# Kernel optimization log

Hardware: AMD Instinct MI355X
Metric: run time of the kernel (lower is better)

Reference implementation:

```python
import jax, jax.numpy as jnp
import numpy as np

FP8_MAX = 448.0  # max finite value of float8_e4m3fn


def _fp8_quant(v, scale):
    # emulate saturating scaled cast to float8_e4m3fn, then dequant-free fp8 storage (upcast to f32 for the gemm)
    q = jnp.clip(v / scale, -FP8_MAX, FP8_MAX)
    return q.astype(jnp.float8_e4m3fn).astype(jnp.float32)


def setup_inputs() -> dict:
    key = jax.random.key(0)
    k0, k1, k2, k3 = jax.random.split(key, 4)
    T, H, I, E = 1024, 1024, 2816, 8
    x = jax.random.normal(k0, (T, H), jnp.float32)
    router_logits = jax.random.normal(k1, (T, E), jnp.float32)
    w13_weight = jax.random.normal(k2, (E, 2 * I, H), jnp.float32) * 0.02
    w2_weight = jax.random.normal(k3, (E, H, I), jnp.float32) * 0.02
    return {
        "x": x,
        "router_logits": router_logits,
        "w13_weight": w13_weight,
        "w2_weight": w2_weight,
        "w13_input_scale": jnp.ones((E,), jnp.float32),
        "w2_input_scale": jnp.ones((E,), jnp.float32),
        "top_k": 2,
    }


def reference(x, router_logits, w13_weight, w2_weight, w13_input_scale, w2_input_scale, top_k):
    T, H = x.shape
    E, two_I, _ = w13_weight.shape
    I = two_I // 2

    # --- routing: softmax -> top_k -> renormalize (select_experts) ---
    probs = jax.nn.softmax(router_logits, axis=-1)
    topk_w, topk_ids = jax.lax.top_k(probs, top_k)            # [T,K]
    topk_w = topk_w / jnp.sum(topk_w, axis=-1, keepdims=True)
    # dense combine matrix [T,E]: sparsity of the grouped gemm dispatch
    combine = jnp.zeros((T, E), x.dtype).at[jnp.arange(T)[:, None], topk_ids].add(topk_w)

    # --- per-expert fp8 weight quantization (ops.scaled_fp8_quant per expert) ---
    w13_scale = jnp.max(jnp.abs(w13_weight), axis=(1, 2)) / FP8_MAX  # [E]
    w2_scale = jnp.max(jnp.abs(w2_weight), axis=(1, 2)) / FP8_MAX
    w13_q = _fp8_quant(w13_weight, w13_scale[:, None, None])         # [E,2I,H]
    w2_q = _fp8_quant(w2_weight, w2_scale[:, None, None])            # [E,H,I]

    # --- grouped gemm 1: per-expert activation quant + fp8 gemm + dequant scale ---
    x_q = _fp8_quant(x[None], w13_input_scale[:, None, None])        # [E,T,H]
    h = jnp.einsum('eth,eih->eti', x_q, w13_q) * (w13_input_scale * w13_scale)[:, None, None]

    # --- silu_and_mul: gate = first intermediate_size rows, up = second ---
    act = jax.nn.silu(h[..., :I]) * h[..., I:]                       # [E,T,I]

    # --- grouped gemm 2 ---
    act_q = _fp8_quant(act, w2_input_scale[:, None, None])
    o = jnp.einsum('eti,ehi->eth', act_q, w2_q) * (w2_input_scale * w2_scale)[:, None, None]

    # --- post_reorder: weighted combine of selected experts ---
    return jnp.einsum('te,eth->th', combine, o)                      # [T,H]
```

## Files before the change

kernel.cpp:

```cpp
#include <hip/hip_runtime.h>
#include <cstdint>
#include <cstddef>

#define T_TOK 1024
#define H_DIM 1024
#define I_DIM 2816
#define E_NUM 8
#define PAIRS 2048
#define KSPLIT 4
#define NT1 (I_DIM / 32)
#define AMX2_X 32

typedef __attribute__((ext_vector_type(4))) float f32x4;
typedef __attribute__((ext_vector_type(4))) unsigned int u32x4;
typedef long i64;

__device__ __forceinline__ unsigned char fp8e4m3_sw(float v) {
  v = fminf(448.f, fmaxf(-448.f, v));
  unsigned b = __float_as_uint(v);
  unsigned s = (b >> 24) & 0x80u;
  float a = fabsf(v);
  if (a < 0.015625f) {
    int m = (int)rintf(a * 512.f);
    return (unsigned char)(s | (unsigned)m);
  }
  unsigned ab = b & 0x7fffffffu;
  unsigned rnd = 0x7FFFFu + ((ab >> 20) & 1u);
  ab += rnd;
  int e = (int)(ab >> 23) - 127;
  unsigned m = (ab >> 20) & 7u;
  if (e > 8 || (e == 8 && m > 6)) { e = 8; m = 6; }
  return (unsigned char)(s | (unsigned)((e + 7) << 3) | m);
}

__device__ __forceinline__ unsigned q4(float a, float b, float c, float d) {
#if __has_builtin(__builtin_amdgcn_cvt_pk_fp8_f32)
  unsigned w = (unsigned)__builtin_amdgcn_cvt_pk_fp8_f32(a, b, 0, false);
  return (unsigned)__builtin_amdgcn_cvt_pk_fp8_f32(c, d, (int)w, true);
#else
  return (unsigned)fp8e4m3_sw(a) | ((unsigned)fp8e4m3_sw(b) << 8) |
         ((unsigned)fp8e4m3_sw(c) << 16) | ((unsigned)fp8e4m3_sw(d) << 24);
#endif
}

__device__ __forceinline__ unsigned char q1(float a) {
#if __has_builtin(__builtin_amdgcn_cvt_pk_fp8_f32)
  return (unsigned char)((unsigned)__builtin_amdgcn_cvt_pk_fp8_f32(a, a, 0, false) & 0xFFu);
#else
  return fp8e4m3_sw(a);
#endif
}

__device__ __forceinline__ unsigned q4v(float4 f, float inv) {
  return q4(f.x * inv, f.y * inv, f.z * inv, f.w * inv);
}

__device__ __forceinline__ float wave_max(float m) {
#pragma unroll
  for (int off = 32; off > 0; off >>= 1) m = fmaxf(m, __shfl_xor(m, off));
  return m;
}

__global__ __launch_bounds__(256) void pre_k(const float* __restrict__ w13,
                                             const float* __restrict__ logits,
                                             float* __restrict__ part13,
                                             int* __restrict__ cnt_g,
                                             int* __restrict__ offs_g,
                                             int* __restrict__ pair_tok,
                                             float* __restrict__ pair_w,
                                             int* __restrict__ pairidx) {
  const int tid = threadIdx.x;
  if (blockIdx.x < 1024) {
    const int e = blockIdx.x >> 7, sub = blockIdx.x & 127;
    const float4* src = (const float4*)w13 + (size_t)e * (2 * I_DIM * H_DIM / 4);
    int idx = sub * 256 + tid;
    const int stride = 128 * 256;
    float m = 0.f;
#pragma unroll
    for (int j = 0; j < 44; j += 4) {
      float4 v0 = src[idx + (size_t)(j + 0) * stride];
      float4 v1 = src[idx + (size_t)(j + 1) * stride];
      float4 v2 = src[idx + (size_t)(j + 2) * stride];
      float4 v3 = src[idx + (size_t)(j + 3) * stride];
      m = fmaxf(m, fmaxf(fmaxf(fabsf(v0.x), fabsf(v0.y)), fmaxf(fabsf(v0.z), fabsf(v0.w))));
      m = fmaxf(m, fmaxf(fmaxf(fabsf(v1.x), fabsf(v1.y)), fmaxf(fabsf(v1.z), fabsf(v1.w))));
      m = fmaxf(m, fmaxf(fmaxf(fabsf(v2.x), fabsf(v2.y)), fmaxf(fabsf(v2.z), fabsf(v2.w))));
      m = fmaxf(m, fmaxf(fmaxf(fabsf(v3.x), fabsf(v3.y)), fmaxf(fabsf(v3.z), fabsf(v3.w))));
    }
    m = wave_max(m);
    __shared__ float wmax[4];
    int lane = tid & 63, wid = tid >> 6;
    if (lane == 0) wmax[wid] = m;
    __syncthreads();
    if (tid == 0)
      part13[blockIdx.x] = fmaxf(fmaxf(wmax[0], wmax[1]), fmaxf(wmax[2], wmax[3]));
    return;
  }

  __shared__ int cnt_s[E_NUM], pos_s[E_NUM];
  if (tid < E_NUM) cnt_s[tid] = 0;
  __syncthreads();
  int i0s[4], i1s[4];
  float w0s[4], w1s[4];
#pragma unroll
  for (int j = 0; j < 4; j++) {
    int t = tid * 4 + j;
    float l[E_NUM];
#pragma unroll
    for (int k = 0; k < E_NUM; k++) l[k] = logits[t * E_NUM + k];
    int i0 = 0; float b0 = l[0];
#pragma unroll
    for (int k = 1; k < E_NUM; k++) { if (l[k] > b0) { b0 = l[k]; i0 = k; } }
    int i1 = -1; float b1 = -3.4e38f;
#pragma unroll
    for (int k = 0; k < E_NUM; k++) { if (k != i0 && l[k] > b1) { b1 = l[k]; i1 = k; } }
    float e1 = expf(b1 - b0);
    float d = 1.f + e1;
    i0s[j] = i0; i1s[j] = i1; w0s[j] = 1.f / d; w1s[j] = e1 / d;
    atomicAdd(&cnt_s[i0], 1);
    atomicAdd(&cnt_s[i1], 1);
  }
  __syncthreads();
  if (tid == 0) {
    int s = 0;
#pragma unroll
    for (int e = 0; e < E_NUM; e++) {
      cnt_g[e] = cnt_s[e];
      offs_g[e] = s;
      pos_s[e] = s;
      s += cnt_s[e];
    }
    offs_g[E_NUM] = s;
  }
  __syncthreads();
#pragma unroll
  for (int j = 0; j < 4; j++) {
    int t = tid * 4 + j;
    int s0 = atomicAdd(&pos_s[i0s[j]], 1);
    pair_tok[s0] = t; pair_w[s0] = w0s[j]; pairidx[2 * t] = s0;
    int s1 = atomicAdd(&pos_s[i1s[j]], 1);
    pair_tok[s1] = t; pair_w[s1] = w1s[j]; pairidx[2 * t + 1] = s1;
  }
}

__global__ __launch_bounds__(256) void quantx_k(const float* __restrict__ x,
                                                const int* __restrict__ pair_tok,
                                                const int* __restrict__ offs,
                                                const float* __restrict__ s13,
                                                unsigned char* __restrict__ Xq) {
  int p = blockIdx.x;
  int t = pair_tok[p];
  int e = 0;
#pragma unroll
  for (int j = 1; j < E_NUM; j++) { if (p >= offs[j]) e = j; }
  float inv = 1.f / s13[e];
  float4 v = ((const float4*)(x + (size_t)t * H_DIM))[threadIdx.x];
  float a = fminf(448.f, fmaxf(-448.f, v.x * inv));
  float b = fminf(448.f, fmaxf(-448.f, v.y * inv));
  float c = fminf(448.f, fmaxf(-448.f, v.z * inv));
  float dd = fminf(448.f, fmaxf(-448.f, v.w * inv));
  ((unsigned*)(Xq + (size_t)p * H_DIM))[threadIdx.x] = q4(a, b, c, dd);
}

__global__ __launch_bounds__(512) void gemm1_k(const float* __restrict__ w13,
                                               const float* __restrict__ w2,
                                               const unsigned char* __restrict__ Xq,
                                               unsigned char* __restrict__ H1,
                                               const int* __restrict__ cnt,
                                               const int* __restrict__ offs,
                                               const float* __restrict__ part13,
                                               float* __restrict__ part2,
                                               const float* __restrict__ s13,
                                               const float* __restrict__ s2in) {
  const int e = blockIdx.z;
  const int tid = threadIdx.x, lane = tid & 63, wq = tid >> 6;

  if (blockIdx.x >= NT1) {
    const int bx2 = (blockIdx.x - NT1) * 4 + blockIdx.y;
    const float4* src = (const float4*)w2 + (size_t)e * (H_DIM * I_DIM / 4);
    int idx = bx2 * 512 + tid;
    const int stride = 128 * 512;
    float m = 0.f;
#pragma unroll
    for (int j = 0; j < 11; j++) {
      float4 v = src[idx + (size_t)j * stride];
      m = fmaxf(m, fmaxf(fmaxf(fabsf(v.x), fabsf(v.y)), fmaxf(fabsf(v.z), fabsf(v.w))));
    }
    m = wave_max(m);
    __shared__ float wmax2[8];
    if (lane == 0) wmax2[wq] = m;
    __syncthreads();
    if (tid == 0) {
      float mm = wmax2[0];
#pragma unroll
      for (int j = 1; j < 8; j++) mm = fmaxf(mm, wmax2[j]);
      part2[e * 128 + bx2] = mm;
    }
    return;
  }

  __shared__ float redA[8];
  {
    float v = part13[e * 128 + (tid & 127)];
    v = wave_max(v);
    if (lane == 0) redA[wq] = v;
  }
  __syncthreads();
  float amax = redA[0];
#pragma unroll
  for (int j = 1; j < 8; j++) amax = fmaxf(amax, redA[j]);

  const int count = cnt[e];
  const int m0 = blockIdx.y * 256;
  if (m0 >= count) return;
  const int nt = blockIdx.x;
  const int base = offs[e];

  const float inv_w = 448.f / amax;
  const float gs = s13[e] * (amax / 448.f);
  const float inv_a2 = 1.f / s2in[e];

  __shared__ __align__(16) unsigned char Bs[64][80];

  const int fr = lane & 15, ks = lane >> 4;

  f32x4 accg[2][2], accu[2][2];
#pragma unroll
  for (int i = 0; i < 2; i++)
#pragma unroll
    for (int j = 0; j < 2; j++) { accg[i][j] = (f32x4)0.f; accu[i][j] = (f32x4)0.f; }

  int rbse = base + m0 + wq * 32 + fr;
  int r0 = rbse;      if (r0 > PAIRS - 1) r0 = PAIRS - 1;
  int r1 = rbse + 16; if (r1 > PAIRS - 1) r1 = PAIRS - 1;
  const unsigned char* a0p = Xq + (size_t)r0 * H_DIM + ks * 8;
  const unsigned char* a1p = Xq + (size_t)r1 * H_DIM + ks * 8;

  const int brow = tid >> 3, bseg = tid & 7;
  const float* b_src = w13 + ((size_t)e * 2 * I_DIM + (size_t)nt * 32 +
                              (brow & 31) + (size_t)(brow >> 5) * I_DIM) * H_DIM + bseg * 8;

  float4 fb0 = ((const float4*)b_src)[0], fb1 = ((const float4*)b_src)[1];
  unsigned qb0 = q4v(fb0, inv_w), qb1 = q4v(fb1, inv_w);
  i64 a00 = *(const i64*)a0p,        a01 = *(const i64*)(a0p + 32);
  i64 a10 = *(const i64*)a1p,        a11 = *(const i64*)(a1p + 32);

  for (int t = 0; t < H_DIM / 64; ++t) {
    __syncthreads();
    ((unsigned*)&Bs[brow][bseg * 8])[0] = qb0;
    ((unsigned*)&Bs[brow][bseg * 8])[1] = qb1;
    __syncthreads();
    i64 c00 = a00, c01 = a01, c10 = a10, c11 = a11;
    if (t + 1 < H_DIM / 64) {
      int k0 = (t + 1) * 64;
      fb0 = ((const float4*)(b_src + k0))[0];
      fb1 = ((const float4*)(b_src + k0))[1];
      a00 = *(const i64*)(a0p + k0); a01 = *(const i64*)(a0p + k0 + 32);
      a10 = *(const i64*)(a1p + k0); a11 = *(const i64*)(a1p + k0 + 32);
    }
#pragma unroll
    for (int kk = 0; kk < 2; kk++) {
      i64 af0 = kk ? c01 : c00;
      i64 af1 = kk ? c11 : c10;
#pragma unroll
      for (int ni = 0; ni < 2; ni++) {
        i64 bg = *(const i64*)&Bs[ni * 16 + fr][kk * 32 + ks * 8];
        i64 bu = *(const i64*)&Bs[32 + ni * 16 + fr][kk * 32 + ks * 8];
        accg[0][ni] = __builtin_amdgcn_mfma_f32_16x16x32_fp8_fp8(af0, bg, accg[0][ni], 0, 0, 0);
        accg[1][ni] = __builtin_amdgcn_mfma_f32_16x16x32_fp8_fp8(af1, bg, accg[1][ni], 0, 0, 0);
        accu[0][ni] = __builtin_amdgcn_mfma_f32_16x16x32_fp8_fp8(af0, bu, accu[0][ni], 0, 0, 0);
        accu[1][ni] = __builtin_amdgcn_mfma_f32_16x16x32_fp8_fp8(af1, bu, accu[1][ni], 0, 0, 0);
      }
    }
    qb0 = q4v(fb0, inv_w);
    qb1 = q4v(fb1, inv_w);
  }

  const int rg = lane >> 4;
#pragma unroll
  for (int mi = 0; mi < 2; mi++) {
#pragma unroll
    for (int rr = 0; rr < 4; rr++) {
      int lrow = wq * 32 + mi * 16 + rg * 4 + rr;
      if (m0 + lrow < count) {
        size_t p = (size_t)(base + m0 + lrow);
#pragma unroll
        for (int ni = 0; ni < 2; ni++) {
          int col = nt * 32 + ni * 16 + fr;
          float g = accg[mi][ni][rr] * gs;
          float u = accu[mi][ni][rr] * gs;
          float act = g / (1.f + expf(-g)) * u * inv_a2;
          act = fminf(448.f, fmaxf(-448.f, act));
          H1[p * I_DIM + col] = q1(act);
        }
      }
    }
  }
}

__global__ __launch_bounds__(512) void gemm2_k(const float* __restrict__ w2,
                                               const unsigned char* __restrict__ H1,
                                               float* __restrict__ Op,
                                               const int* __restrict__ cnt,
                                               const int* __restrict__ offs,
                                               const float* __restrict__ part2,
                                               const float* __restrict__ s2in,
                                               const float* __restrict__ pair_w) {
  const int e = blockIdx.z;
  const int tid = threadIdx.x, lane = tid & 63, wq = tid >> 6;

  __shared__ float redA[8];
  {
    float v = part2[e * 128 + (tid & 127)];
    v = wave_max(v);
    if (lane == 0) redA[wq] = v;
  }
  __syncthreads();
  float amax = redA[0];
#pragma unroll
  for (int j = 1; j < 8; j++) amax = fmaxf(amax, redA[j]);

  const int count = cnt[e];
  const int m0 = blockIdx.y * 128;
  if (m0 >= count) return;
  const int nt = blockIdx.x & 15;
  const int ksp = blockIdx.x >> 4;
  const int n0 = nt * 64;
  const int base = offs[e];

  const float inv_w = 448.f / amax;
  const float s2 = s2in[e] * (amax / 448.f);

  __shared__ __align__(16) unsigned char Bs[64][80];

  const int fr = lane & 15, ks = lane >> 4;

  f32x4 acc[4];
#pragma unroll
  for (int i = 0; i < 4; i++) acc[i] = (f32x4)0.f;

  const int KITER = (I_DIM / 64) / KSPLIT;
  const int kbase = ksp * KITER * 64;

  int rbse = base + m0 + wq * 16 + fr;
  int r0 = rbse; if (r0 > PAIRS - 1) r0 = PAIRS - 1;
  const unsigned char* ap = H1 + (size_t)r0 * I_DIM + kbase + ks * 8;

  const int brow = tid >> 3, bseg = tid & 7;
  const float* b_src = w2 + ((size_t)e * H_DIM + n0 + brow) * I_DIM + kbase + bseg * 8;

  float4 fb0 = ((const float4*)b_src)[0], fb1 = ((const float4*)b_src)[1];
  unsigned qb0 = q4v(fb0, inv_w), qb1 = q4v(fb1, inv_w);
  i64 a0 = *(const i64*)ap, a1 = *(const i64*)(ap + 32);

  for (int t = 0; t < KITER; ++t) {
    __syncthreads();
    ((unsigned*)&Bs[brow][bseg * 8])[0] = qb0;
    ((unsigned*)&Bs[brow][bseg * 8])[1] = qb1;
    __syncthreads();
    i64 c0 = a0, c1 = a1;
    if (t + 1 < KITER) {
      int k0 = (t + 1) * 64;
      fb0 = ((const float4*)(b_src + k0))[0];
      fb1 = ((const float4*)(b_src + k0))[1];
      a0 = *(const i64*)(ap + k0); a1 = *(const i64*)(ap + k0 + 32);
    }
#pragma unroll
    for (int kk = 0; kk < 2; kk++) {
      i64 af = kk ? c1 : c0;
#pragma unroll
      for (int ni = 0; ni < 4; ni++) {
        i64 b = *(const i64*)&Bs[ni * 16 + fr][kk * 32 + ks * 8];
        acc[ni] = __builtin_amdgcn_mfma_f32_16x16x32_fp8_fp8(af, b, acc[ni], 0, 0, 0);
      }
    }
    qb0 = q4v(fb0, inv_w);
    qb1 = q4v(fb1, inv_w);
  }

  const int rg = lane >> 4;
#pragma unroll
  for (int rr = 0; rr < 4; rr++) {
    int lrow = wq * 16 + rg * 4 + rr;
    if (m0 + lrow < count) {
      size_t p = (size_t)(base + m0 + lrow);
      float pw = pair_w[p];
#pragma unroll
      for (int ni = 0; ni < 4; ni++) {
        int col = n0 + ni * 16 + fr;
        Op[((size_t)ksp * PAIRS + p) * H_DIM + col] = acc[ni][rr] * s2 * pw;
      }
    }
  }
}

__global__ __launch_bounds__(256) void combine_k(const float* __restrict__ Op,
                                                 const int* __restrict__ pairidx,
                                                 float* __restrict__ out) {
  int t = blockIdx.x;
  int p0 = pairidx[2 * t], p1 = pairidx[2 * t + 1];
  f32x4 acc = (f32x4)0.f;
#pragma unroll
  for (int s = 0; s < KSPLIT; s++) {
    f32x4 a = ((const f32x4*)(Op + ((size_t)s * PAIRS + p0) * H_DIM))[threadIdx.x];
    f32x4 b = ((const f32x4*)(Op + ((size_t)s * PAIRS + p1) * H_DIM))[threadIdx.x];
    acc += a + b;
  }
  ((f32x4*)(out + (size_t)t * H_DIM))[threadIdx.x] = acc;
}

extern "C" void kernel_launch(void* const* d_in, const int* in_sizes, int n_in,
                              void* d_out, int out_size, void* d_ws, size_t ws_size,
                              hipStream_t stream) {
  (void)in_sizes; (void)n_in; (void)out_size; (void)ws_size;
  const float* x      = (const float*)d_in[0];
  const float* logits = (const float*)d_in[1];
  const float* w13    = (const float*)d_in[2];
  const float* w2     = (const float*)d_in[3];
  const float* s13    = (const float*)d_in[4];
  const float* s2in   = (const float*)d_in[5];
  float* out = (float*)d_out;

  char* ws = (char*)d_ws;
  int* cnt      = (int*)(ws + 128);
  int* offs     = (int*)(ws + 192);
  float* part13 = (float*)(ws + 4096);
  float* part2  = (float*)(ws + 8192);
  int* pair_tok = (int*)(ws + 17408);
  float* pair_w = (float*)(ws + 25600);
  int* pairidx  = (int*)(ws + 33792);
  unsigned char* Xq = (unsigned char*)(ws + (size_t)(1 << 20));
  unsigned char* H1 = (unsigned char*)(ws + (size_t)4 * (1 << 20));
  float* Op         = (float*)(ws + (size_t)10 * (1 << 20));

  pre_k<<<1025, 256, 0, stream>>>(w13, logits, part13, cnt, offs,
                                  pair_tok, pair_w, pairidx);

  quantx_k<<<PAIRS, 256, 0, stream>>>(x, pair_tok, offs, s13, Xq);

  gemm1_k<<<dim3(NT1 + AMX2_X, 4, E_NUM), 512, 0, stream>>>(
      w13, w2, Xq, H1, cnt, offs, part13, part2, s13, s2in);

  gemm2_k<<<dim3(16 * KSPLIT, 8, E_NUM), 512, 0, stream>>>(
      w2, H1, Op, cnt, offs, part2, s2in, pair_w);

  combine_k<<<T_TOK, 256, 0, stream>>>(Op, pairidx, out);
}
```

Measured before the change: 202.8 us.

## Stage fp8 activations through LDS with coalesced loads and retile gemm1 blocks

Both grouped GEMMs now load the fp8 activation tile cooperatively with 16-byte coalesced global loads into shared memory. They then read MFMA fragments from LDS instead of doing scattered 8-byte per-lane global loads. gemm1 moves to 256-thread blocks covering 128 rows instead of 256, and loads gate and up weights separately. A block-index swizzle places the two M halves of the same N tile next to each other so they can share weight reads in L2. The trade-off is more blocks that re-read and re-quantize fp32 weight tiles, plus extra LDS use and LDS traffic.

```diff
diff --git a/kernel.cpp b/kernel.cpp
--- a/kernel.cpp
+++ b/kernel.cpp
@@ -8,7 +8,7 @@
 #define E_NUM 8
 #define PAIRS 2048
 #define KSPLIT 4
-#define NT1 (I_DIM / 32)
+#define NT1 88
 #define AMX2_X 32
 
 typedef __attribute__((ext_vector_type(4))) float f32x4;
@@ -162,7 +162,7 @@
   ((unsigned*)(Xq + (size_t)p * H_DIM))[threadIdx.x] = q4(a, b, c, dd);
 }
 
-__global__ __launch_bounds__(512) void gemm1_k(const float* __restrict__ w13,
+__global__ __launch_bounds__(256) void gemm1_k(const float* __restrict__ w13,
                                                const float* __restrict__ w2,
                                                const unsigned char* __restrict__ Xq,
                                                unsigned char* __restrict__ H1,
@@ -175,51 +175,50 @@
   const int e = blockIdx.z;
   const int tid = threadIdx.x, lane = tid & 63, wq = tid >> 6;
 
-  if (blockIdx.x >= NT1) {
-    const int bx2 = (blockIdx.x - NT1) * 4 + blockIdx.y;
+  if (blockIdx.x >= 2 * NT1) {
+    const int bx2 = (blockIdx.x - 2 * NT1) * 4 + blockIdx.y;
     const float4* src = (const float4*)w2 + (size_t)e * (H_DIM * I_DIM / 4);
-    int idx = bx2 * 512 + tid;
-    const int stride = 128 * 512;
+    int idx = bx2 * 256 + tid;
+    const int stride = 128 * 256;
     float m = 0.f;
 #pragma unroll
-    for (int j = 0; j < 11; j++) {
+    for (int j = 0; j < 22; j++) {
       float4 v = src[idx + (size_t)j * stride];
       m = fmaxf(m, fmaxf(fmaxf(fabsf(v.x), fabsf(v.y)), fmaxf(fabsf(v.z), fabsf(v.w))));
     }
     m = wave_max(m);
-    __shared__ float wmax2[8];
+    __shared__ float wmax2[4];
     if (lane == 0) wmax2[wq] = m;
     __syncthreads();
     if (tid == 0) {
-      float mm = wmax2[0];
-#pragma unroll
-      for (int j = 1; j < 8; j++) mm = fmaxf(mm, wmax2[j]);
+      float mm = fmaxf(fmaxf(wmax2[0], wmax2[1]), fmaxf(wmax2[2], wmax2[3]));
       part2[e * 128 + bx2] = mm;
     }
     return;
   }
 
-  __shared__ float redA[8];
+  __shared__ float redA[4];
   {
     float v = part13[e * 128 + (tid & 127)];
     v = wave_max(v);
     if (lane == 0) redA[wq] = v;
   }
   __syncthreads();
-  float amax = redA[0];
-#pragma unroll
-  for (int j = 1; j < 8; j++) amax = fmaxf(amax, redA[j]);
-
+  float amax = fmaxf(fmaxf(redA[0], redA[1]), fmaxf(redA[2], redA[3]));
+
+  const int bid = blockIdx.x;
+  const int nt = (bid & 7) + (bid >> 4) * 8;
+  const int mhalf = (bid >> 3) & 1;
+  const int m0 = (blockIdx.y * 2 + mhalf) * 128;
   const int count = cnt[e];
-  const int m0 = blockIdx.y * 256;
   if (m0 >= count) return;
-  const int nt = blockIdx.x;
   const int base = offs[e];
 
   const float inv_w = 448.f / amax;
   const float gs = s13[e] * (amax / 448.f);
   const float inv_a2 = 1.f / s2in[e];
 
+  __shared__ __align__(16) unsigned char As[128][80];
   __shared__ __align__(16) unsigned char Bs[64][80];
 
   const int fr = lane & 15, ks = lane >> 4;
@@ -230,50 +229,59 @@
 #pragma unroll
     for (int j = 0; j < 2; j++) { accg[i][j] = (f32x4)0.f; accu[i][j] = (f32x4)0.f; }
 
-  int rbse = base + m0 + wq * 32 + fr;
-  int r0 = rbse;      if (r0 > PAIRS - 1) r0 = PAIRS - 1;
-  int r1 = rbse + 16; if (r1 > PAIRS - 1) r1 = PAIRS - 1;
-  const unsigned char* a0p = Xq + (size_t)r0 * H_DIM + ks * 8;
-  const unsigned char* a1p = Xq + (size_t)r1 * H_DIM + ks * 8;
+  const int ar0 = tid >> 2, aseg = tid & 3;
+  int pr0 = base + m0 + ar0;      if (pr0 > PAIRS - 1) pr0 = PAIRS - 1;
+  int pr1 = base + m0 + ar0 + 64; if (pr1 > PAIRS - 1) pr1 = PAIRS - 1;
+  const unsigned char* a_src0 = Xq + (size_t)pr0 * H_DIM + aseg * 16;
+  const unsigned char* a_src1 = Xq + (size_t)pr1 * H_DIM + aseg * 16;
 
   const int brow = tid >> 3, bseg = tid & 7;
-  const float* b_src = w13 + ((size_t)e * 2 * I_DIM + (size_t)nt * 32 +
-                              (brow & 31) + (size_t)(brow >> 5) * I_DIM) * H_DIM + bseg * 8;
-
-  float4 fb0 = ((const float4*)b_src)[0], fb1 = ((const float4*)b_src)[1];
-  unsigned qb0 = q4v(fb0, inv_w), qb1 = q4v(fb1, inv_w);
-  i64 a00 = *(const i64*)a0p,        a01 = *(const i64*)(a0p + 32);
-  i64 a10 = *(const i64*)a1p,        a11 = *(const i64*)(a1p + 32);
+  const float* bg_src = w13 + ((size_t)e * 2 * I_DIM + (size_t)nt * 32 + brow) * H_DIM + bseg * 8;
+  const float* bu_src = bg_src + (size_t)I_DIM * H_DIM;
+
+  u32x4 ra0 = *(const u32x4*)a_src0;
+  u32x4 ra1 = *(const u32x4*)a_src1;
+  float4 fg0 = ((const float4*)bg_src)[0], fg1 = ((const float4*)bg_src)[1];
+  float4 fu0 = ((const float4*)bu_src)[0], fu1 = ((const float4*)bu_src)[1];
+  unsigned qg0 = q4v(fg0, inv_w), qg1 = q4v(fg1, inv_w);
+  unsigned qu0 = q4v(fu0, inv_w), qu1 = q4v(fu1, inv_w);
 
   for (int t = 0; t < H_DIM / 64; ++t) {
     __syncthreads();
-    ((unsigned*)&Bs[brow][bseg * 8])[0] = qb0;
-    ((unsigned*)&Bs[brow][bseg * 8])[1] = qb1;
-    __syncthreads();
-    i64 c00 = a00, c01 = a01, c10 = a10, c11 = a11;
+    *(u32x4*)&As[ar0][aseg * 16] = ra0;
+    *(u32x4*)&As[ar0 + 64][aseg * 16] = ra1;
+    ((unsigned*)&Bs[brow][bseg * 8])[0] = qg0;
+    ((unsigned*)&Bs[brow][bseg * 8])[1] = qg1;
+    ((unsigned*)&Bs[32 + brow][bseg * 8])[0] = qu0;
+    ((unsigned*)&Bs[32 + brow][bseg * 8])[1] = qu1;
+    __syncthreads();
     if (t + 1 < H_DIM / 64) {
       int k0 = (t + 1) * 64;
-      fb0 = ((const float4*)(b_src + k0))[0];
-      fb1 = ((const float4*)(b_src + k0))[1];
-      a00 = *(const i64*)(a0p + k0); a01 = *(const i64*)(a0p + k0 + 32);
-      a10 = *(const i64*)(a1p + k0); a11 = *(const i64*)(a1p + k0 + 32);
+      ra0 = *(const u32x4*)(a_src0 + k0);
+      ra1 = *(const u32x4*)(a_src1 + k0);
+      fg0 = ((const float4*)(bg_src + k0))[0];
+      fg1 = ((const float4*)(bg_src + k0))[1];
+      fu0 = ((const float4*)(bu_src + k0))[0];
+      fu1 = ((const float4*)(bu_src + k0))[1];
     }
 #pragma unroll
     for (int kk = 0; kk < 2; kk++) {
-      i64 af0 = kk ? c01 : c00;
-      i64 af1 = kk ? c11 : c10;
+      i64 a0 = *(const i64*)&As[wq * 32 + fr][kk * 32 + ks * 8];
+      i64 a1 = *(const i64*)&As[wq * 32 + 16 + fr][kk * 32 + ks * 8];
 #pragma unroll
       for (int ni = 0; ni < 2; ni++) {
         i64 bg = *(const i64*)&Bs[ni * 16 + fr][kk * 32 + ks * 8];
         i64 bu = *(const i64*)&Bs[32 + ni * 16 + fr][kk * 32 + ks * 8];
-        accg[0][ni] = __builtin_amdgcn_mfma_f32_16x16x32_fp8_fp8(af0, bg, accg[0][ni], 0, 0, 0);
-        accg[1][ni] = __builtin_amdgcn_mfma_f32_16x16x32_fp8_fp8(af1, bg, accg[1][ni], 0, 0, 0);
-        accu[0][ni] = __builtin_amdgcn_mfma_f32_16x16x32_fp8_fp8(af0, bu, accu[0][ni], 0, 0, 0);
-        accu[1][ni] = __builtin_amdgcn_mfma_f32_16x16x32_fp8_fp8(af1, bu, accu[1][ni], 0, 0, 0);
+        accg[0][ni] = __builtin_amdgcn_mfma_f32_16x16x32_fp8_fp8(a0, bg, accg[0][ni], 0, 0, 0);
+        accg[1][ni] = __builtin_amdgcn_mfma_f32_16x16x32_fp8_fp8(a1, bg, accg[1][ni], 0, 0, 0);
+        accu[0][ni] = __builtin_amdgcn_mfma_f32_16x16x32_fp8_fp8(a0, bu, accu[0][ni], 0, 0, 0);
+        accu[1][ni] = __builtin_amdgcn_mfma_f32_16x16x32_fp8_fp8(a1, bu, accu[1][ni], 0, 0, 0);
       }
     }
-    qb0 = q4v(fb0, inv_w);
-    qb1 = q4v(fb1, inv_w);
+    qg0 = q4v(fg0, inv_w);
+    qg1 = q4v(fg1, inv_w);
+    qu0 = q4v(fu0, inv_w);
+    qu1 = q4v(fu1, inv_w);
   }
 
   const int rg = lane >> 4;
@@ -331,6 +339,7 @@
   const float inv_w = 448.f / amax;
   const float s2 = s2in[e] * (amax / 448.f);
 
+  __shared__ __align__(16) unsigned char As[128][80];
   __shared__ __align__(16) unsigned char Bs[64][80];
 
   const int fr = lane & 15, ks = lane >> 4;
@@ -338,40 +347,41 @@
   f32x4 acc[4];
 #pragma unroll
   for (int i = 0; i < 4; i++) acc[i] = (f32x4)0.f;
+
+  const int arow = tid >> 2, aseg = tid & 3;
+  int pr = base + m0 + arow; if (pr > PAIRS - 1) pr = PAIRS - 1;
+  const unsigned char* a_src = H1 + (size_t)pr * I_DIM + aseg * 16;
+
+  const int brow = tid >> 3, bseg = tid & 7;
+  const float* b_src = w2 + ((size_t)e * H_DIM + n0 + brow) * I_DIM + bseg * 8;
 
   const int KITER = (I_DIM / 64) / KSPLIT;
   const int kbase = ksp * KITER * 64;
 
-  int rbse = base + m0 + wq * 16 + fr;
-  int r0 = rbse; if (r0 > PAIRS - 1) r0 = PAIRS - 1;
-  const unsigned char* ap = H1 + (size_t)r0 * I_DIM + kbase + ks * 8;
-
-  const int brow = tid >> 3, bseg = tid & 7;
-  const float* b_src = w2 + ((size_t)e * H_DIM + n0 + brow) * I_DIM + kbase + bseg * 8;
-
-  float4 fb0 = ((const float4*)b_src)[0], fb1 = ((const float4*)b_src)[1];
+  u32x4 ra = *(const u32x4*)(a_src + kbase);
+  float4 fb0 = ((const float4*)(b_src + kbase))[0];
+  float4 fb1 = ((const float4*)(b_src + kbase))[1];
   unsigned qb0 = q4v(fb0, inv_w), qb1 = q4v(fb1, inv_w);
-  i64 a0 = *(const i64*)ap, a1 = *(const i64*)(ap + 32);
 
   for (int t = 0; t < KITER; ++t) {
     __syncthreads();
+    *(u32x4*)&As[arow][aseg * 16] = ra;
     ((unsigned*)&Bs[brow][bseg * 8])[0] = qb0;
     ((unsigned*)&Bs[brow][bseg * 8])[1] = qb1;
     __syncthreads();
-    i64 c0 = a0, c1 = a1;
     if (t + 1 < KITER) {
-      int k0 = (t + 1) * 64;
+      int k0 = kbase + (t + 1) * 64;
+      ra = *(const u32x4*)(a_src + k0);
       fb0 = ((const float4*)(b_src + k0))[0];
       fb1 = ((const float4*)(b_src + k0))[1];
-      a0 = *(const i64*)(ap + k0); a1 = *(const i64*)(ap + k0 + 32);
     }
 #pragma unroll
     for (int kk = 0; kk < 2; kk++) {
-      i64 af = kk ? c1 : c0;
+      i64 a0 = *(const i64*)&As[wq * 16 + fr][kk * 32 + ks * 8];
 #pragma unroll
       for (int ni = 0; ni < 4; ni++) {
         i64 b = *(const i64*)&Bs[ni * 16 + fr][kk * 32 + ks * 8];
-        acc[ni] = __builtin_amdgcn_mfma_f32_16x16x32_fp8_fp8(af, b, acc[ni], 0, 0, 0);
+        acc[ni] = __builtin_amdgcn_mfma_f32_16x16x32_fp8_fp8(a0, b, acc[ni], 0, 0, 0);
       }
     }
     qb0 = q4v(fb0, inv_w);
@@ -438,7 +448,7 @@
 
   quantx_k<<<PAIRS, 256, 0, stream>>>(x, pair_tok, offs, s13, Xq);
 
-  gemm1_k<<<dim3(NT1 + AMX2_X, 4, E_NUM), 512, 0, stream>>>(
+  gemm1_k<<<dim3(2 * NT1 + AMX2_X, 4, E_NUM), 256, 0, stream>>>(
       w13, w2, Xq, H1, cnt, offs, part13, part2, s13, s2in);
 
   gemm2_k<<<dim3(16 * KSPLIT, 8, E_NUM), 512, 0, stream>>>(
```

Measured after the change: 170.3 us. -16.0%, faster.

## Fuse x quantization into routing kernel and stage GEMM A tiles in LDS

Applied to the files above, without the earlier changes.

Removes the separate quantx_k launch. Extra blocks in pre_k recompute top-2 per token and write each token's two quantized copies at token-ordered rows. gemm1 then gathers those rows through a pair_xrow index. Both GEMMs now load A tiles cooperatively with 16-byte global loads into shared memory instead of per-lane 8-byte global loads, trading extra LDS traffic and occupancy for coalesced access and one fewer launch.

```diff
diff --git a/kernel.cpp b/kernel.cpp
--- a/kernel.cpp
+++ b/kernel.cpp
@@ -8,7 +8,7 @@
 #define E_NUM 8
 #define PAIRS 2048
 #define KSPLIT 4
-#define NT1 (I_DIM / 32)
+#define NT1 88
 #define AMX2_X 32
 
 typedef __attribute__((ext_vector_type(4))) float f32x4;
@@ -55,20 +55,40 @@
   return q4(f.x * inv, f.y * inv, f.z * inv, f.w * inv);
 }
 
+__device__ __forceinline__ unsigned q4c(float4 f, float inv) {
+  float a = fminf(448.f, fmaxf(-448.f, f.x * inv));
+  float b = fminf(448.f, fmaxf(-448.f, f.y * inv));
+  float c = fminf(448.f, fmaxf(-448.f, f.z * inv));
+  float d = fminf(448.f, fmaxf(-448.f, f.w * inv));
+  return q4(a, b, c, d);
+}
+
 __device__ __forceinline__ float wave_max(float m) {
 #pragma unroll
   for (int off = 32; off > 0; off >>= 1) m = fmaxf(m, __shfl_xor(m, off));
   return m;
 }
 
+__device__ __forceinline__ void top2(const float* l, int& i0, int& i1) {
+  i0 = 0; float b0 = l[0];
+#pragma unroll
+  for (int k = 1; k < E_NUM; k++) { if (l[k] > b0) { b0 = l[k]; i0 = k; } }
+  i1 = -1; float b1 = -3.4e38f;
+#pragma unroll
+  for (int k = 0; k < E_NUM; k++) { if (k != i0 && l[k] > b1) { b1 = l[k]; i1 = k; } }
+}
+
 __global__ __launch_bounds__(256) void pre_k(const float* __restrict__ w13,
                                              const float* __restrict__ logits,
+                                             const float* __restrict__ x,
+                                             const float* __restrict__ s13,
                                              float* __restrict__ part13,
                                              int* __restrict__ cnt_g,
                                              int* __restrict__ offs_g,
-                                             int* __restrict__ pair_tok,
+                                             int* __restrict__ pair_xrow,
                                              float* __restrict__ pair_w,
-                                             int* __restrict__ pairidx) {
+                                             int* __restrict__ pairidx,
+                                             unsigned char* __restrict__ Xq) {
   const int tid = threadIdx.x;
   if (blockIdx.x < 1024) {
     const int e = blockIdx.x >> 7, sub = blockIdx.x & 127;
@@ -97,69 +117,67 @@
     return;
   }
 
-  __shared__ int cnt_s[E_NUM], pos_s[E_NUM];
-  if (tid < E_NUM) cnt_s[tid] = 0;
-  __syncthreads();
-  int i0s[4], i1s[4];
-  float w0s[4], w1s[4];
-#pragma unroll
-  for (int j = 0; j < 4; j++) {
-    int t = tid * 4 + j;
-    float l[E_NUM];
-#pragma unroll
-    for (int k = 0; k < E_NUM; k++) l[k] = logits[t * E_NUM + k];
-    int i0 = 0; float b0 = l[0];
-#pragma unroll
-    for (int k = 1; k < E_NUM; k++) { if (l[k] > b0) { b0 = l[k]; i0 = k; } }
-    int i1 = -1; float b1 = -3.4e38f;
-#pragma unroll
-    for (int k = 0; k < E_NUM; k++) { if (k != i0 && l[k] > b1) { b1 = l[k]; i1 = k; } }
-    float e1 = expf(b1 - b0);
-    float d = 1.f + e1;
-    i0s[j] = i0; i1s[j] = i1; w0s[j] = 1.f / d; w1s[j] = e1 / d;
-    atomicAdd(&cnt_s[i0], 1);
-    atomicAdd(&cnt_s[i1], 1);
-  }
-  __syncthreads();
-  if (tid == 0) {
-    int s = 0;
-#pragma unroll
-    for (int e = 0; e < E_NUM; e++) {
-      cnt_g[e] = cnt_s[e];
-      offs_g[e] = s;
-      pos_s[e] = s;
-      s += cnt_s[e];
-    }
-    offs_g[E_NUM] = s;
-  }
-  __syncthreads();
-#pragma unroll
-  for (int j = 0; j < 4; j++) {
-    int t = tid * 4 + j;
-    int s0 = atomicAdd(&pos_s[i0s[j]], 1);
-    pair_tok[s0] = t; pair_w[s0] = w0s[j]; pairidx[2 * t] = s0;
-    int s1 = atomicAdd(&pos_s[i1s[j]], 1);
-    pair_tok[s1] = t; pair_w[s1] = w1s[j]; pairidx[2 * t + 1] = s1;
-  }
-}
-
-__global__ __launch_bounds__(256) void quantx_k(const float* __restrict__ x,
-                                                const int* __restrict__ pair_tok,
-                                                const int* __restrict__ offs,
-                                                const float* __restrict__ s13,
-                                                unsigned char* __restrict__ Xq) {
-  int p = blockIdx.x;
-  int t = pair_tok[p];
-  int e = 0;
-#pragma unroll
-  for (int j = 1; j < E_NUM; j++) { if (p >= offs[j]) e = j; }
-  float inv = 1.f / s13[e];
-  float4 v = ((const float4*)(x + (size_t)t * H_DIM))[threadIdx.x];
-  float a = fminf(448.f, fmaxf(-448.f, v.x * inv));
-  float b = fminf(448.f, fmaxf(-448.f, v.y * inv));
-  float c = fminf(448.f, fmaxf(-448.f, v.z * inv));
-  float dd = fminf(448.f, fmaxf(-448.f, v.w * inv));
-  ((unsigned*)(Xq + (size_t)p * H_DIM))[threadIdx.x] = q4(a, b, c, dd);
+  if (blockIdx.x == 1024) {
+    __shared__ int cnt_s[E_NUM], pos_s[E_NUM];
+    if (tid < E_NUM) cnt_s[tid] = 0;
+    __syncthreads();
+    int i0s[4], i1s[4];
+    float w0s[4], w1s[4];
+#pragma unroll
+    for (int j = 0; j < 4; j++) {
+      int t = tid * 4 + j;
+      float l[E_NUM];
+#pragma unroll
+      for (int k = 0; k < E_NUM; k++) l[k] = logits[t * E_NUM + k];
+      int i0, i1;
+      top2(l, i0, i1);
+      float e1 = expf(l[i1] - l[i0]);
+      float d = 1.f + e1;
+      i0s[j] = i0; i1s[j] = i1; w0s[j] = 1.f / d; w1s[j] = e1 / d;
+      atomicAdd(&cnt_s[i0], 1);
+      atomicAdd(&cnt_s[i1], 1);
+    }
+    __syncthreads();
+    if (tid == 0) {
+      int s = 0;
+#pragma unroll
+      for (int e = 0; e < E_NUM; e++) {
+        cnt_g[e] = cnt_s[e];
+        offs_g[e] = s;
+        pos_s[e] = s;
+        s += cnt_s[e];
+      }
+      offs_g[E_NUM] = s;
+    }
+    __syncthreads();
+#pragma unroll
+    for (int j = 0; j < 4; j++) {
+      int t = tid * 4 + j;
+      int s0 = atomicAdd(&pos_s[i0s[j]], 1);
+      pair_xrow[s0] = 2 * t; pair_w[s0] = w0s[j]; pairidx[2 * t] = s0;
+      int s1 = atomicAdd(&pos_s[i1s[j]], 1);
+      pair_xrow[s1] = 2 * t + 1; pair_w[s1] = w1s[j]; pairidx[2 * t + 1] = s1;
+    }
+    return;
+  }
+
+  {
+    const int q = blockIdx.x - 1025;
+#pragma unroll
+    for (int j = 0; j < 2; j++) {
+      int t = q * 2 + j;
+      float l[E_NUM];
+#pragma unroll
+      for (int k = 0; k < E_NUM; k++) l[k] = logits[t * E_NUM + k];
+      int i0, i1;
+      top2(l, i0, i1);
+      float inv0 = 1.f / s13[i0];
+      float inv1 = 1.f / s13[i1];
+      float4 v = ((const float4*)(x + (size_t)t * H_DIM))[tid];
+      ((unsigned*)(Xq + (size_t)(2 * t) * H_DIM))[tid] = q4c(v, inv0);
+      ((unsigned*)(Xq + (size_t)(2 * t + 1) * H_DIM))[tid] = q4c(v, inv1);
+    }
+  }
 }
 
 __global__ __launch_bounds__(512) void gemm1_k(const float* __restrict__ w13,
@@ -170,6 +188,7 @@
                                                const int* __restrict__ offs,
                                                const float* __restrict__ part13,
                                                float* __restrict__ part2,
+                                               const int* __restrict__ pair_xrow,
                                                const float* __restrict__ s13,
                                                const float* __restrict__ s2in) {
   const int e = blockIdx.z;
@@ -220,6 +239,7 @@
   const float gs = s13[e] * (amax / 448.f);
   const float inv_a2 = 1.f / s2in[e];
 
+  __shared__ __align__(16) unsigned char As[256][80];
   __shared__ __align__(16) unsigned char Bs[64][80];
 
   const int fr = lane & 15, ks = lane >> 4;
@@ -230,46 +250,47 @@
 #pragma unroll
     for (int j = 0; j < 2; j++) { accg[i][j] = (f32x4)0.f; accu[i][j] = (f32x4)0.f; }
 
-  int rbse = base + m0 + wq * 32 + fr;
-  int r0 = rbse;      if (r0 > PAIRS - 1) r0 = PAIRS - 1;
-  int r1 = rbse + 16; if (r1 > PAIRS - 1) r1 = PAIRS - 1;
-  const unsigned char* a0p = Xq + (size_t)r0 * H_DIM + ks * 8;
-  const unsigned char* a1p = Xq + (size_t)r1 * H_DIM + ks * 8;
+  const int ar0 = tid >> 2, aseg = tid & 3;
+  int pr0 = base + m0 + ar0;       if (pr0 > PAIRS - 1) pr0 = PAIRS - 1;
+  int pr1 = base + m0 + ar0 + 128; if (pr1 > PAIRS - 1) pr1 = PAIRS - 1;
+  const unsigned char* a_src0 = Xq + (size_t)pair_xrow[pr0] * H_DIM + aseg * 16;
+  const unsigned char* a_src1 = Xq + (size_t)pair_xrow[pr1] * H_DIM + aseg * 16;
 
   const int brow = tid >> 3, bseg = tid & 7;
-  const float* b_src = w13 + ((size_t)e * 2 * I_DIM + (size_t)nt * 32 +
-                              (brow & 31) + (size_t)(brow >> 5) * I_DIM) * H_DIM + bseg * 8;
-
+  const size_t brg = (size_t)nt * 32 + (brow & 31) + (size_t)(brow >> 5) * I_DIM;
+  const float* b_src = w13 + ((size_t)e * 2 * I_DIM + brg) * H_DIM + bseg * 8;
+
+  u32x4 ra0 = *(const u32x4*)a_src0;
+  u32x4 ra1 = *(const u32x4*)a_src1;
   float4 fb0 = ((const float4*)b_src)[0], fb1 = ((const float4*)b_src)[1];
   unsigned qb0 = q4v(fb0, inv_w), qb1 = q4v(fb1, inv_w);
-  i64 a00 = *(const i64*)a0p,        a01 = *(const i64*)(a0p + 32);
-  i64 a10 = *(const i64*)a1p,        a11 = *(const i64*)(a1p + 32);
 
   for (int t = 0; t < H_DIM / 64; ++t) {
     __syncthreads();
+    *(u32x4*)&As[ar0][aseg * 16] = ra0;
+    *(u32x4*)&As[ar0 + 128][aseg * 16] = ra1;
     ((unsigned*)&Bs[brow][bseg * 8])[0] = qb0;
     ((unsigned*)&Bs[brow][bseg * 8])[1] = qb1;
     __syncthreads();
-    i64 c00 = a00, c01 = a01, c10 = a10, c11 = a11;
     if (t + 1 < H_DIM / 64) {
       int k0 = (t + 1) * 64;
+      ra0 = *(const u32x4*)(a_src0 + k0);
+      ra1 = *(const u32x4*)(a_src1 + k0);
       fb0 = ((const float4*)(b_src + k0))[0];
       fb1 = ((const float4*)(b_src + k0))[1];
-      a00 = *(const i64*)(a0p + k0); a01 = *(const i64*)(a0p + k0 + 32);
-      a10 = *(const i64*)(a1p + k0); a11 = *(const i64*)(a1p + k0 + 32);
     }
 #pragma unroll
     for (int kk = 0; kk < 2; kk++) {
-      i64 af0 = kk ? c01 : c00;
-      i64 af1 = kk ? c11 : c10;
+      i64 a0 = *(const i64*)&As[wq * 32 + fr][kk * 32 + ks * 8];
+      i64 a1 = *(const i64*)&As[wq * 32 + 16 + fr][kk * 32 + ks * 8];
 #pragma unroll
       for (int ni = 0; ni < 2; ni++) {
         i64 bg = *(const i64*)&Bs[ni * 16 + fr][kk * 32 + ks * 8];
         i64 bu = *(const i64*)&Bs[32 + ni * 16 + fr][kk * 32 + ks * 8];
-        accg[0][ni] = __builtin_amdgcn_mfma_f32_16x16x32_fp8_fp8(af0, bg, accg[0][ni], 0, 0, 0);
-        accg[1][ni] = __builtin_amdgcn_mfma_f32_16x16x32_fp8_fp8(af1, bg, accg[1][ni], 0, 0, 0);
-        accu[0][ni] = __builtin_amdgcn_mfma_f32_16x16x32_fp8_fp8(af0, bu, accu[0][ni], 0, 0, 0);
-        accu[1][ni] = __builtin_amdgcn_mfma_f32_16x16x32_fp8_fp8(af1, bu, accu[1][ni], 0, 0, 0);
+        accg[0][ni] = __builtin_amdgcn_mfma_f32_16x16x32_fp8_fp8(a0, bg, accg[0][ni], 0, 0, 0);
+        accg[1][ni] = __builtin_amdgcn_mfma_f32_16x16x32_fp8_fp8(a1, bg, accg[1][ni], 0, 0, 0);
+        accu[0][ni] = __builtin_amdgcn_mfma_f32_16x16x32_fp8_fp8(a0, bu, accu[0][ni], 0, 0, 0);
+        accu[1][ni] = __builtin_amdgcn_mfma_f32_16x16x32_fp8_fp8(a1, bu, accu[1][ni], 0, 0, 0);
       }
     }
     qb0 = q4v(fb0, inv_w);
@@ -331,6 +352,7 @@
   const float inv_w = 448.f / amax;
   const float s2 = s2in[e] * (amax / 448.f);
 
+  __shared__ __align__(16) unsigned char As[128][80];
   __shared__ __align__(16) unsigned char Bs[64][80];
 
   const int fr = lane & 15, ks = lane >> 4;
@@ -338,40 +360,41 @@
   f32x4 acc[4];
 #pragma unroll
   for (int i = 0; i < 4; i++) acc[i] = (f32x4)0.f;
+
+  const int arow = tid >> 2, aseg = tid & 3;
+  int pr = base + m0 + arow; if (pr > PAIRS - 1) pr = PAIRS - 1;
+  const unsigned char* a_src = H1 + (size_t)pr * I_DIM + aseg * 16;
+
+  const int brow = tid >> 3, bseg = tid & 7;
+  const float* b_src = w2 + ((size_t)e * H_DIM + n0 + brow) * I_DIM + bseg * 8;
 
   const int KITER = (I_DIM / 64) / KSPLIT;
   const int kbase = ksp * KITER * 64;
 
-  int rbse = base + m0 + wq * 16 + fr;
-  int r0 = rbse; if (r0 > PAIRS - 1) r0 = PAIRS - 1;
-  const unsigned char* ap = H1 + (size_t)r0 * I_DIM + kbase + ks * 8;
-
-  const int brow = tid >> 3, bseg = tid & 7;
-  const float* b_src = w2 + ((size_t)e * H_DIM + n0 + brow) * I_DIM + kbase + bseg * 8;
-
-  float4 fb0 = ((const float4*)b_src)[0], fb1 = ((const float4*)b_src)[1];
+  u32x4 ra = *(const u32x4*)(a_src + kbase);
+  float4 fb0 = ((const float4*)(b_src + kbase))[0];
+  float4 fb1 = ((const float4*)(b_src + kbase))[1];
   unsigned qb0 = q4v(fb0, inv_w), qb1 = q4v(fb1, inv_w);
-  i64 a0 = *(const i64*)ap, a1 = *(const i64*)(ap + 32);
 
   for (int t = 0; t < KITER; ++t) {
     __syncthreads();
+    *(u32x4*)&As[arow][aseg * 16] = ra;
     ((unsigned*)&Bs[brow][bseg * 8])[0] = qb0;
     ((unsigned*)&Bs[brow][bseg * 8])[1] = qb1;
     __syncthreads();
-    i64 c0 = a0, c1 = a1;
     if (t + 1 < KITER) {
-      int k0 = (t + 1) * 64;
+      int k0 = kbase + (t + 1) * 64;
+      ra = *(const u32x4*)(a_src + k0);
       fb0 = ((const float4*)(b_src + k0))[0];
       fb1 = ((const float4*)(b_src + k0))[1];
-      a0 = *(const i64*)(ap + k0); a1 = *(const i64*)(ap + k0 + 32);
     }
 #pragma unroll
     for (int kk = 0; kk < 2; kk++) {
-      i64 af = kk ? c1 : c0;
+      i64 a0 = *(const i64*)&As[wq * 16 + fr][kk * 32 + ks * 8];
 #pragma unroll
       for (int ni = 0; ni < 4; ni++) {
         i64 b = *(const i64*)&Bs[ni * 16 + fr][kk * 32 + ks * 8];
-        acc[ni] = __builtin_amdgcn_mfma_f32_16x16x32_fp8_fp8(af, b, acc[ni], 0, 0, 0);
+        acc[ni] = __builtin_amdgcn_mfma_f32_16x16x32_fp8_fp8(a0, b, acc[ni], 0, 0, 0);
       }
     }
     qb0 = q4v(fb0, inv_w);
@@ -422,24 +445,22 @@
   float* out = (float*)d_out;
 
   char* ws = (char*)d_ws;
-  int* cnt      = (int*)(ws + 128);
-  int* offs     = (int*)(ws + 192);
-  float* part13 = (float*)(ws + 4096);
-  float* part2  = (float*)(ws + 8192);
-  int* pair_tok = (int*)(ws + 17408);
-  float* pair_w = (float*)(ws + 25600);
-  int* pairidx  = (int*)(ws + 33792);
+  int* cnt       = (int*)(ws + 128);
+  int* offs      = (int*)(ws + 192);
+  float* part13  = (float*)(ws + 4096);
+  float* part2   = (float*)(ws + 8192);
+  int* pair_xrow = (int*)(ws + 17408);
+  float* pair_w  = (float*)(ws + 25600);
+  int* pairidx   = (int*)(ws + 33792);
   unsigned char* Xq = (unsigned char*)(ws + (size_t)(1 << 20));
   unsigned char* H1 = (unsigned char*)(ws + (size_t)4 * (1 << 20));
   float* Op         = (float*)(ws + (size_t)10 * (1 << 20));
 
-  pre_k<<<1025, 256, 0, stream>>>(w13, logits, part13, cnt, offs,
-                                  pair_tok, pair_w, pairidx);
-
-  quantx_k<<<PAIRS, 256, 0, stream>>>(x, pair_tok, offs, s13, Xq);
+  pre_k<<<1537, 256, 0, stream>>>(w13, logits, x, s13, part13, cnt, offs,
+                                  pair_xrow, pair_w, pairidx, Xq);
 
   gemm1_k<<<dim3(NT1 + AMX2_X, 4, E_NUM), 512, 0, stream>>>(
-      w13, w2, Xq, H1, cnt, offs, part13, part2, s13, s2in);
+      w13, w2, Xq, H1, cnt, offs, part13, part2, pair_xrow, s13, s2in);
 
   gemm2_k<<<dim3(16 * KSPLIT, 8, E_NUM), 512, 0, stream>>>(
       w2, H1, Op, cnt, offs, part2, s2in, pair_w);
```

Measured after the change: 164.8 us. -18.7%, faster.
